# Performance work log

Measured on AMD Instinct MI355X. Metric: run time of the kernel, lower is better.

Reference implementation:

```python
import jax, jax.numpy as jnp
import numpy as np

B, L, C, H, W = 2, 4, 64, 80, 80
DISCRETE_RATIO, DOWNSAMPLE_RATE, NUM_ITER = 0.4, 2, 2


def _conv2d(x, w, b):
    y = jax.lax.conv_general_dilated(x, w, (1, 1), 'SAME',
                                     dimension_numbers=('NCHW', 'OIHW', 'NCHW'))
    return y + b[None, :, None, None]


def _get_transformation_matrix(M, h, w):
    # shift(center) @ [R 0; 0 1] @ shift(-center), then add raw translation (kornia-style)
    R = M[:, :2, :2]
    center = jnp.array([w / 2.0, h / 2.0], M.dtype)
    trans = center[None, :] - jnp.einsum('nij,j->ni', R, center) + M[:, :, 2]
    return jnp.concatenate([R, trans[:, :, None]], axis=2)  # (N,2,3)


def _warp_affine(src, M, mode):
    # src (N,C,h,w); M (N,2,3) maps src pixels -> dst pixels; sample src at M^{-1} @ dst
    # (equivalent to F.affine_grid/grid_sample with align_corners=True, zeros padding)
    N, Cc, h, w = src.shape
    bottom = jnp.tile(jnp.array([[[0.0, 0.0, 1.0]]], src.dtype), (N, 1, 1))
    Minv = jnp.linalg.inv(jnp.concatenate([M, bottom], axis=1))
    yy, xx = jnp.meshgrid(jnp.arange(h, dtype=src.dtype),
                          jnp.arange(w, dtype=src.dtype), indexing='ij')
    pts = jnp.stack([xx.ravel(), yy.ravel(), jnp.ones(h * w, src.dtype)], 0)  # (3,P)
    sp = jnp.einsum('nij,jp->nip', Minv, pts)
    sx, sy = sp[:, 0], sp[:, 1]  # (N,P) source pixel coords
    flat = src.reshape(N, Cc, h * w)

    def gather(ix, iy):
        valid = ((ix >= 0) & (ix < w) & (iy >= 0) & (iy < h)).astype(src.dtype)
        idx = jnp.clip(iy, 0, h - 1) * w + jnp.clip(ix, 0, w - 1)
        vals = jnp.take_along_axis(flat, jnp.broadcast_to(idx[:, None, :], (N, Cc, h * w)), axis=2)
        return vals * valid[:, None, :]

    if mode == 'nearest':
        out = gather(jnp.round(sx).astype(jnp.int32), jnp.round(sy).astype(jnp.int32))
    else:
        x0 = jnp.floor(sx); y0 = jnp.floor(sy)
        fx = (sx - x0)[:, None, :]; fy = (sy - y0)[:, None, :]
        x0 = x0.astype(jnp.int32); y0 = y0.astype(jnp.int32)
        out = (gather(x0, y0) * (1 - fx) * (1 - fy)
               + gather(x0 + 1, y0) * fx * (1 - fy)
               + gather(x0, y0 + 1) * (1 - fx) * fy
               + gather(x0 + 1, y0 + 1) * fx * fy)
    return out.reshape(N, Cc, h, w)


def _forward(x, pairwise_t_matrix, msg_w, msg_b, gates_w, gates_b, can_w, can_b, mlp_w, mlp_b):
    feats = x.reshape(B, L, C, H, W)
    # rows [0,1], cols [0,1,3] of the 4x4 SE(3) matrices; discretize translation
    t = pairwise_t_matrix[..., :2, :][..., jnp.array([0, 1, 3])]  # (B,L,L,2,3)
    t = t.at[..., 2].set(t[..., 2] / (DISCRETE_RATIO * DOWNSAMPLE_RATE))
    T = _get_transformation_matrix(t.reshape(-1, 2, 3), H, W)  # (B*L*L,2,3), flat index (b, j, i)
    mask = _warp_affine(jnp.ones((B * L * L, 1, H, W), x.dtype), T, 'nearest').reshape(B, L, L, 1, H, W)

    for _ in range(NUM_ITER):
        # 'b c h w -> b c w h' + flip(last): coordinate-convention fix (H==W)
        y = jnp.flip(jnp.swapaxes(feats, -1, -2), axis=-1)  # (B,L,C,H,W)
        # warp neighbor j into ego i frame with T[b,j,i]
        src = jnp.broadcast_to(y[:, :, None], (B, L, L, C, H, W)).reshape(-1, C, H, W)
        neighbor = _warp_affine(src, T, 'bilinear')
        ego = jnp.broadcast_to(y[:, None], (B, L, L, C, H, W)).reshape(-1, C, H, W)
        msg = _conv2d(jnp.concatenate([neighbor, ego], axis=1), msg_w, msg_b)
        msg = msg.reshape(B, L, L, C, H, W) * mask
        agg = msg.mean(axis=1)  # 'avg' over neighbors j -> (B,L,C,H,W)
        cat_feat = jnp.concatenate([y, agg], axis=2).reshape(B * L, 2 * C, H, W)
        # single ConvGRU step with zero initial hidden state
        h0 = jnp.zeros((B * L, C, H, W), x.dtype)
        gates = _conv2d(jnp.concatenate([cat_feat, h0], axis=1), gates_w, gates_b)
        reset = jax.nn.sigmoid(gates[:, :C])
        update = jax.nn.sigmoid(gates[:, C:])
        cand = jnp.tanh(_conv2d(jnp.concatenate([cat_feat, reset * h0], axis=1), can_w, can_b))
        h1 = (1.0 - update) * h0 + update * cand
        # undo the coordinate fix: flip(last) then 'c w h -> c h w'
        feats = jnp.swapaxes(jnp.flip(h1.reshape(B, L, C, H, W), axis=-1), -1, -2)

    out = feats[:, 0]  # ego agent of each sample, (B,C,H,W)
    return jnp.einsum('bchw,oc->bhwo', out, mlp_w) + mlp_b  # nn.Linear on channel-last


def setup_inputs() -> dict:
    key = jax.random.key(0)
    ks = jax.random.split(key, 12)
    x = jax.random.normal(ks[0], (B * L, C, H, W), dtype=jnp.float32)
    record_len = jnp.full((B,), L, dtype=jnp.int32)
    # realistic SE(2) pairwise transforms embedded in 4x4 homogeneous matrices
    ang = jax.random.uniform(ks[1], (B, L, L), minval=-0.3, maxval=0.3)
    tx = jax.random.uniform(ks[2], (B, L, L), minval=-8.0, maxval=8.0)
    ty = jax.random.uniform(ks[3], (B, L, L), minval=-8.0, maxval=8.0)
    c, s = jnp.cos(ang), jnp.sin(ang)
    z, o = jnp.zeros_like(ang), jnp.ones_like(ang)
    pairwise_t_matrix = jnp.stack([c, -s, z, tx,
                                   s, c, z, ty,
                                   z, z, o, z,
                                   z, z, z, o], axis=-1).reshape(B, L, L, 4, 4).astype(jnp.float32)
    prior_encoding = jax.random.normal(ks[4], (B * L, 3), dtype=jnp.float32)  # unused by forward
    sc = 0.05
    return {
        'x': x,
        'record_len': record_len,
        'pairwise_t_matrix': pairwise_t_matrix,
        'prior_encoding': prior_encoding,
        'msg_w': jax.random.normal(ks[5], (C, 2 * C, 3, 3), dtype=jnp.float32) * sc,
        'msg_b': jnp.zeros((C,), jnp.float32),
        'gates_w': jax.random.normal(ks[6], (2 * C, 3 * C, 3, 3), dtype=jnp.float32) * sc,
        'gates_b': jnp.zeros((2 * C,), jnp.float32),
        'can_w': jax.random.normal(ks[7], (C, 3 * C, 3, 3), dtype=jnp.float32) * sc,
        'can_b': jnp.zeros((C,), jnp.float32),
        'mlp_w': jax.random.normal(ks[8], (C, C), dtype=jnp.float32) * sc,
        'mlp_b': jnp.zeros((C,), jnp.float32),
    }


def reference(x, record_len, pairwise_t_matrix, prior_encoding,
              msg_w, msg_b, gates_w, gates_b, can_w, can_b, mlp_w, mlp_b):
    # record_len is fixed to L for every sample; prior_encoding is unused by the torch forward
    return _forward(x, pairwise_t_matrix, msg_w, msg_b, gates_w, gates_b,
                    can_w, can_b, mlp_w, mlp_b)
```

## Files before the change

kernel.cpp:

```cpp
#include <hip/hip_runtime.h>
#include <math.h>

#define WD 80
#define HW 6400
#define PW 82
#define PPX 6790
#define NIMG 8
#define NPAIR 32
#define TSTG 960

typedef short bf16x8 __attribute__((ext_vector_type(8)));
typedef float f32x4 __attribute__((ext_vector_type(4)));

__device__ __forceinline__ float bf2f(unsigned short u) {
    return __uint_as_float(((unsigned)u) << 16);
}
__device__ __forceinline__ unsigned short f2bf(float f) {
    unsigned u = __float_as_uint(f);
    u += 0x7fff + ((u >> 16) & 1);
    return (unsigned short)(u >> 16);
}

__device__ __forceinline__ void inv_affine(const float* __restrict__ P, int p, float* a) {
    const float* m = P + p * 16;
    float m00 = m[0], m01 = m[1], m02 = m[3] / 0.8f;
    float m10 = m[4], m11 = m[5], m12 = m[7] / 0.8f;
    float cx = 40.0f, cy = 40.0f;
    float tx = cx - (m00 * cx + m01 * cy) + m02;
    float ty = cy - (m10 * cx + m11 * cy) + m12;
    float id = 1.0f / (m00 * m11 - m01 * m10);
    a[0] =  m11 * id; a[1] = -m01 * id;
    a[3] = -m10 * id; a[4] =  m00 * id;
    a[2] = -(a[0] * tx + a[1] * ty);
    a[5] = -(a[3] * tx + a[4] * ty);
}

__global__ __launch_bounds__(256) void prologue_all(
        const float* __restrict__ P, float* __restrict__ mats, float* __restrict__ mask,
        const float* __restrict__ msg_w, const float* __restrict__ gates_w,
        const float* __restrict__ can_w,
        unsigned short* __restrict__ Wn, unsigned short* __restrict__ We,
        unsigned short* __restrict__ Wu, unsigned short* __restrict__ Wc,
        const float* __restrict__ x, unsigned short* __restrict__ bufs) {
    __shared__ float T[64][81];
    int bx = blockIdx.x;
    if (bx < 243) {
        int idx = bx * 256 + threadIdx.x;
        if (idx >= 24 * 324 * 8) return;
        int g = idx & 7;
        int e = (idx >> 3) % 324;
        int img = idx / (324 * 8);
        int pp;
        if (e < 82)       pp = e;
        else if (e < 164) pp = 81 * PW + (e - 82);
        else if (e < 244) pp = (e - 164 + 1) * PW;
        else              pp = (e - 244 + 1) * PW + 81;
        *(uint4*)(bufs + ((size_t)img * PPX + pp) * 64 + g * 8) = (uint4){0, 0, 0, 0};
        return;
    }
    bx -= 243;
    if (bx < 32) {
        int p = bx;
        float a[6];
        inv_affine(P, p, a);
        if (threadIdx.x < 6) mats[p * 6 + threadIdx.x] = a[threadIdx.x];
        for (int q = threadIdx.x; q < HW; q += blockDim.x) {
            float xx = (float)(q % WD), yy = (float)(q / WD);
            float sx = a[0] * xx + a[1] * yy + a[2];
            float sy = a[3] * xx + a[4] * yy + a[5];
            int ix = (int)rintf(sx), iy = (int)rintf(sy);
            mask[p * HW + q] = (ix >= 0 && ix < WD && iy >= 0 && iy < WD) ? 1.0f : 0.0f;
        }
        return;
    }
    bx -= 32;
    if (bx < 864) {
        int t = bx * 256 + threadIdx.x;
        if (t >= 221184) return;
        const float* src; unsigned short* dst;
        int cin_n, co_off, ci_off, stride, u;
        if (t < 36864)       { src = msg_w;   dst = Wn; cin_n = 64;  co_off = 0;  ci_off = 0;  stride = 1152; u = t; }
        else if (t < 73728)  { src = msg_w;   dst = We; cin_n = 64;  co_off = 0;  ci_off = 64; stride = 1152; u = t - 36864; }
        else if (t < 147456) { src = gates_w; dst = Wu; cin_n = 128; co_off = 64; ci_off = 0;  stride = 1728; u = t - 73728; }
        else                 { src = can_w;   dst = Wc; cin_n = 128; co_off = 0;  ci_off = 0;  stride = 1728; u = t - 147456; }
        int ci = u % cin_n;
        int co = (u / cin_n) & 63;
        int tap = u / (cin_n * 64);
        dst[u] = f2bf(src[(size_t)(co_off + co) * stride + (ci_off + ci) * 9 + tap]);
        return;
    }
    bx -= 864;
    int img = bx / 80, hh = bx % 80;
    int tid = threadIdx.x;
    for (int idx = tid; idx < 64 * 80; idx += 256) {
        int c = idx / 80, ww = idx % 80;
        T[c][ww] = x[((size_t)(img * 64 + c) * 80 + hh) * 80 + ww];
    }
    __syncthreads();
    int b = 79 - hh;
    for (int idx = tid; idx < 80 * 64; idx += 256) {
        int a = idx >> 6, ch = idx & 63;
        bufs[((size_t)img * PPX + (a + 1) * PW + (b + 1)) * 64 + ch] = f2bf(T[ch][a]);
    }
}

__device__ __forceinline__ void stage_t(const unsigned short* __restrict__ src,
                                        int x0, int y0, uint4* bufbase, int tid) {
    const int lane = tid & 63;
    const int wv = tid >> 6;
    for (int c = wv; c < TSTG / 64; c += 4) {
        int s = c * 64 + lane;
        int q = s >> 3;
        int yl = q / 20, xl = q - yl * 20;
        int g = (s & 7) ^ (q & 7);
        const unsigned short* gp = src + ((y0 + yl) * PW + x0 + xl) * 64 + g * 8;
        __builtin_amdgcn_global_load_lds(
            (const __attribute__((address_space(1))) unsigned int*)gp,
            (__attribute__((address_space(3))) unsigned int*)(bufbase + c * 64),
            16, 0, 0);
    }
}

__device__ __forceinline__ void stage_warp(const unsigned short* __restrict__ src,
        const float* __restrict__ am, int x0, int y0, uint4* bufbase, int tid) {
    float a0 = am[0], a1 = am[1], a2 = am[2], a3 = am[3], a4 = am[4], a5 = am[5];
    for (int idx = tid; idx < TSTG; idx += 256) {
        int q = idx >> 3, g = idx & 7;
        int yl = q / 20, xl = q - yl * 20;
        int ux = x0 + xl - 1, uy = y0 + yl - 1;
        uint4 v = {0, 0, 0, 0};
        if ((unsigned)ux < WD && (unsigned)uy < WD) {
            float sx = a0 * ux + a1 * uy + a2;
            float sy = a3 * ux + a4 * uy + a5;
            float fxf = floorf(sx), fyf = floorf(sy);
            float fx = sx - fxf, fy = sy - fyf;
            int ix = (int)fxf, iy = (int)fyf;
            float w00 = (1.f - fx) * (1.f - fy), w10 = fx * (1.f - fy);
            float w01 = (1.f - fx) * fy,         w11 = fx * fy;
            bool vx0 = (unsigned)ix < WD, vx1 = (unsigned)(ix + 1) < WD;
            bool vy0 = (unsigned)iy < WD, vy1 = (unsigned)(iy + 1) < WD;
            if (!(vx0 && vy0)) w00 = 0.f;
            if (!(vx1 && vy0)) w10 = 0.f;
            if (!(vx0 && vy1)) w01 = 0.f;
            if (!(vx1 && vy1)) w11 = 0.f;
            int cx0 = min(max(ix, 0), WD - 1), cx1 = min(max(ix + 1, 0), WD - 1);
            int cy0 = min(max(iy, 0), WD - 1), cy1 = min(max(iy + 1, 0), WD - 1);
            const unsigned short* s8 = src + g * 8;
            uint4 c00 = *(const uint4*)(s8 + ((cy0 + 1) * PW + cx0 + 1) * 64);
            uint4 c10 = *(const uint4*)(s8 + ((cy0 + 1) * PW + cx1 + 1) * 64);
            uint4 c01 = *(const uint4*)(s8 + ((cy1 + 1) * PW + cx0 + 1) * 64);
            uint4 c11 = *(const uint4*)(s8 + ((cy1 + 1) * PW + cx1 + 1) * 64);
            const unsigned short* p00 = (const unsigned short*)&c00;
            const unsigned short* p10 = (const unsigned short*)&c10;
            const unsigned short* p01 = (const unsigned short*)&c01;
            const unsigned short* p11 = (const unsigned short*)&c11;
            unsigned short r8[8];
#pragma unroll
            for (int kk = 0; kk < 8; ++kk) {
                float vv = w00 * bf2f(p00[kk]) + w10 * bf2f(p10[kk])
                         + w01 * bf2f(p01[kk]) + w11 * bf2f(p11[kk]);
                r8[kk] = f2bf(vv);
            }
            v = *(const uint4*)r8;
        }
        bufbase[q * 8 + (g ^ (q & 7))] = v;
    }
}

__device__ __forceinline__ void load_w(const unsigned short* __restrict__ W, int row,
                                       int cinstride, int cin0, int lh, bf16x8* Wf) {
#pragma unroll
    for (int ks = 0; ks < 2; ++ks)
#pragma unroll
        for (int tap = 0; tap < 9; ++tap)
            Wf[ks * 9 + tap] = *(const bf16x8*)(W + (size_t)(tap * 64 + row) * cinstride
                                                + cin0 + ks * 32 + lh * 8);
}

__device__ __forceinline__ void conv_pass4(const uint4* __restrict__ buf, const bf16x8* Wf,
                                           int ll, int lh, f32x4* acc) {
#pragma unroll
    for (int ks = 0; ks < 2; ++ks) {
        const int g = ks * 4 + lh;
#pragma unroll
        for (int tx = 0; tx < 3; ++tx) {
            bf16x8 A[6];
#pragma unroll
            for (int s = 0; s < 6; ++s) {
                int q = s * 20 + tx + ll;
                A[s] = *(const bf16x8*)&buf[q * 8 + (g ^ (q & 7))];
            }
#pragma unroll
            for (int ty = 0; ty < 3; ++ty) {
                bf16x8 B = Wf[ks * 9 + ty * 3 + tx];
#pragma unroll
                for (int r = 0; r < 4; ++r)
                    acc[r] = __builtin_amdgcn_mfma_f32_16x16x32_bf16(A[r + ty], B, acc[r], 0, 0, 0);
            }
        }
    }
}

__global__ __launch_bounds__(256, 2) void msg_agg(const unsigned short* __restrict__ Y,
        const float* __restrict__ mats, const float* __restrict__ mask,
        const unsigned short* __restrict__ Wn, const unsigned short* __restrict__ We,
        const float* __restrict__ bias, unsigned short* __restrict__ Gpad, int only0) {
    __shared__ uint4 lds[2 * TSTG];
    __shared__ float lmask[4][4][16];
    const int tid = threadIdx.x, lane = tid & 63, wv = tid >> 6;
    const int ll = lane & 15, lh = lane >> 4;
    const int x0 = blockIdx.x * 16, y0 = blockIdx.y * 4;
    const int t = blockIdx.z;
    const int b = only0 ? t : (t >> 2), j = only0 ? 0 : (t & 3);
    const int img = only0 ? t * 4 : t;
    const int row = wv * 16 + ll;

    int ps_[4];
#pragma unroll
    for (int i = 0; i < 4; ++i) {
        int k = only0 ? (b * 4 + i) : ((b * 4 + i) * 4 + j);
        ps_[i] = only0 ? k * 4 : k;
    }
    {
        int i = tid >> 6, r = (tid >> 4) & 3, px = tid & 15;
        lmask[i][r][px] = mask[(size_t)ps_[i] * HW + (y0 + r) * WD + x0 + px];
    }
    bf16x8 Wf[18];
    load_w(Wn, row, 64, 0, lh, Wf);
    stage_warp(Y + (size_t)(b * 4 + 0) * PPX * 64, mats + ps_[0] * 6, x0, y0, lds, tid);
    __syncthreads();

    f32x4 tot[4];
#pragma unroll
    for (int r = 0; r < 4; ++r) tot[r] = (f32x4){0.f, 0.f, 0.f, 0.f};

    for (int i = 0; i < 4; ++i) {
        if (i < 3)
            stage_warp(Y + (size_t)(b * 4 + i + 1) * PPX * 64, mats + ps_[i + 1] * 6,
                       x0, y0, lds + ((i + 1) & 1) * TSTG, tid);
        else
            stage_t(Y + (size_t)img * PPX * 64, x0, y0, lds, tid);
        f32x4 acc[4];
#pragma unroll
        for (int r = 0; r < 4; ++r) acc[r] = (f32x4){0.f, 0.f, 0.f, 0.f};
        conv_pass4(lds + (i & 1) * TSTG, Wf, ll, lh, acc);
#pragma unroll
        for (int r = 0; r < 4; ++r)
#pragma unroll
            for (int jj = 0; jj < 4; ++jj)
                tot[r][jj] += lmask[i][r][lh * 4 + jj] * acc[r][jj];
        __syncthreads();
    }

    load_w(We, row, 64, 0, lh, Wf);
    f32x4 acc[4];
#pragma unroll
    for (int r = 0; r < 4; ++r) acc[r] = (f32x4){0.f, 0.f, 0.f, 0.f};
    conv_pass4(lds, Wf, ll, lh, acc);

    float bv = bias[row];
#pragma unroll
    for (int r = 0; r < 4; ++r)
#pragma unroll
        for (int jj = 0; jj < 4; ++jj) {
            int px = lh * 4 + jj;
            float msum = lmask[0][r][px] + lmask[1][r][px] + lmask[2][r][px] + lmask[3][r][px];
            float val = 0.25f * (tot[r][jj] + msum * (acc[r][jj] + bv));
            Gpad[((size_t)t * PPX + (y0 + r + 1) * PW + (x0 + px + 1)) * 64 + row] = f2bf(val);
        }
}

__global__ __launch_bounds__(256, 2) void gru_conv(const unsigned short* __restrict__ Ysrc,
        const unsigned short* __restrict__ Gpad,
        const unsigned short* __restrict__ Wu, const unsigned short* __restrict__ Wc,
        const float* __restrict__ bu, const float* __restrict__ bc,
        unsigned short* __restrict__ Ydst, int only0) {
    __shared__ uint4 lds[2 * TSTG];
    const int tid = threadIdx.x, lane = tid & 63, wv = tid >> 6;
    const int ll = lane & 15, lh = lane >> 4;
    const int x0 = blockIdx.x * 16, y0 = blockIdx.y * 4;
    const int t = blockIdx.z;
    const int img = only0 ? t * 4 : t;
    const int row = wv * 16 + ll;

    stage_t(Ysrc + (size_t)img * PPX * 64, x0, y0, lds, tid);
    stage_t(Gpad + (size_t)t * PPX * 64, x0, y0, lds + TSTG, tid);
    bf16x8 Wf[18];
    load_w(Wu, row, 128, 0, lh, Wf);
    __syncthreads();

    f32x4 aU[4], aC[4];
#pragma unroll
    for (int r = 0; r < 4; ++r) {
        aU[r] = (f32x4){0.f, 0.f, 0.f, 0.f};
        aC[r] = (f32x4){0.f, 0.f, 0.f, 0.f};
    }
    conv_pass4(lds, Wf, ll, lh, aU);
    load_w(Wu, row, 128, 64, lh, Wf);
    conv_pass4(lds + TSTG, Wf, ll, lh, aU);
    load_w(Wc, row, 128, 0, lh, Wf);
    conv_pass4(lds, Wf, ll, lh, aC);
    load_w(Wc, row, 128, 64, lh, Wf);
    conv_pass4(lds + TSTG, Wf, ll, lh, aC);

    float ub = bu[row], cb = bc[row];
#pragma unroll
    for (int r = 0; r < 4; ++r)
#pragma unroll
        for (int jj = 0; jj < 4; ++jj) {
            int x = x0 + lh * 4 + jj;
            float u = 1.f / (1.f + __expf(-(aU[r][jj] + ub)));
            float e2 = __expf(2.f * (aC[r][jj] + cb));
            float c = (e2 - 1.f) / (e2 + 1.f);
            Ydst[((size_t)img * PPX + (y0 + r + 1) * PW + (x + 1)) * 64 + row] = f2bf(u * c);
        }
}

__global__ void final_mlp(const unsigned short* __restrict__ yfin, const float* __restrict__ mw,
                          const float* __restrict__ mb, float* __restrict__ out) {
    int t = blockIdx.x * blockDim.x + threadIdx.x;
    if (t >= 2 * HW * 64) return;
    int o  = t & 63;
    int wv = (t >> 6) % WD;
    int h  = ((t >> 6) / WD) % WD;
    int b  = t / (HW * 64);
    const unsigned short* src = yfin + ((size_t)(b * 4) * PPX + (wv + 1) * PW + (80 - h)) * 64;
    const float* wrow = mw + o * 64;
    float r = mb[o];
#pragma unroll
    for (int c8 = 0; c8 < 8; ++c8) {
        bf16x8 v = *(const bf16x8*)(src + c8 * 8);
#pragma unroll
        for (int k = 0; k < 8; ++k)
            r += bf2f(((const unsigned short*)&v)[k]) * wrow[c8 * 8 + k];
    }
    out[t] = r;
}

extern "C" void kernel_launch(void* const* d_in, const int* in_sizes, int n_in,
                              void* d_out, int out_size, void* d_ws, size_t ws_size,
                              hipStream_t stream) {
    const float* x       = (const float*)d_in[0];
    const float* P       = (const float*)d_in[2];
    const float* msg_w   = (const float*)d_in[4];
    const float* msg_b   = (const float*)d_in[5];
    const float* gates_w = (const float*)d_in[6];
    const float* gates_b = (const float*)d_in[7];
    const float* can_w   = (const float*)d_in[8];
    const float* can_b   = (const float*)d_in[9];
    const float* mlp_w   = (const float*)d_in[10];
    const float* mlp_b   = (const float*)d_in[11];
    float* out = (float*)d_out;

    char* wsb = (char*)d_ws;
    float* mats = (float*)wsb;
    float* mask = (float*)(wsb + 1024);
    unsigned short* Wn = (unsigned short*)(wsb + 820224);
    unsigned short* We = Wn + 36864;
    unsigned short* Wu = We + 36864;
    unsigned short* Wc = Wu + 73728;
    unsigned short* Y0 = Wc + 73728;
    unsigned short* Y1 = Y0 + (size_t)NIMG * PPX * 64;
    unsigned short* Gpad = Y1 + (size_t)NIMG * PPX * 64;

    prologue_all<<<243 + 32 + 864 + 640, 256, 0, stream>>>(P, mats, mask,
        msg_w, gates_w, can_w, Wn, We, Wu, Wc, x, Y0);

    msg_agg<<<dim3(5, 20, 8), 256, 0, stream>>>(Y0, mats, mask, Wn, We, msg_b, Gpad, 0);
    gru_conv<<<dim3(5, 20, 8), 256, 0, stream>>>(Y0, Gpad, Wu, Wc, gates_b + 64, can_b, Y1, 0);

    msg_agg<<<dim3(5, 20, 2), 256, 0, stream>>>(Y1, mats, mask, Wn, We, msg_b, Gpad, 1);
    gru_conv<<<dim3(5, 20, 2), 256, 0, stream>>>(Y1, Gpad, Wu, Wc, gates_b + 64, can_b, Y0, 1);

    final_mlp<<<(2 * HW * 64 + 255) / 256, 256, 0, stream>>>(Y0, mlp_w, mlp_b, out);
}
```

Measured before the change: 239.5 us.

## Make conv kernels loop over tiles with cross-tile LDS prefetch

msg_agg and gru_conv become grid-stride kernels: the first iteration uses 400 blocks that each process two tiles, and the second uses 200 blocks with one tile each. While the current tile is computing, the next tile's warped neighbour data, mask and inputs are staged into a second LDS buffer, so global loads overlap with MFMA work across tile boundaries. In exchange, gru_conv's LDS doubles, which may lower occupancy, and the first iteration launches fewer blocks, which may leave CUs idle on a chip with many compute units.

After: 307.4 us. +28.4%, slower.

```diff
diff --git a/kernel.cpp b/kernel.cpp
--- a/kernel.cpp
+++ b/kernel.cpp
@@ -101,6 +101,21 @@
     for (int idx = tid; idx < 80 * 64; idx += 256) {
         int a = idx >> 6, ch = idx & 63;
         bufs[((size_t)img * PPX + (a + 1) * PW + (b + 1)) * 64 + ch] = f2bf(T[ch][a]);
+    }
+}
+
+struct TileInfo { int x0, y0, t, b, img; int ps[4]; };
+__device__ __forceinline__ void decode_tile(int tt, int only0, TileInfo& ti) {
+    int bx = tt % 5, by = (tt / 5) % 20;
+    ti.t = tt / 100;
+    ti.x0 = bx * 16; ti.y0 = by * 4;
+    int b = only0 ? ti.t : (ti.t >> 2), j = only0 ? 0 : (ti.t & 3);
+    ti.b = b;
+    ti.img = only0 ? ti.t * 4 : ti.t;
+#pragma unroll
+    for (int i = 0; i < 4; ++i) {
+        int k = only0 ? (b * 4 + i) : ((b * 4 + i) * 4 + j);
+        ti.ps[i] = only0 ? k * 4 : k;
     }
 }
 
@@ -204,116 +219,144 @@
 __global__ __launch_bounds__(256, 2) void msg_agg(const unsigned short* __restrict__ Y,
         const float* __restrict__ mats, const float* __restrict__ mask,
         const unsigned short* __restrict__ Wn, const unsigned short* __restrict__ We,
-        const float* __restrict__ bias, unsigned short* __restrict__ Gpad, int only0) {
+        const float* __restrict__ bias, unsigned short* __restrict__ Gpad,
+        int total, int nt, int only0) {
     __shared__ uint4 lds[2 * TSTG];
-    __shared__ float lmask[4][4][16];
+    __shared__ float lmask[2][4][4][16];
     const int tid = threadIdx.x, lane = tid & 63, wv = tid >> 6;
     const int ll = lane & 15, lh = lane >> 4;
-    const int x0 = blockIdx.x * 16, y0 = blockIdx.y * 4;
-    const int t = blockIdx.z;
-    const int b = only0 ? t : (t >> 2), j = only0 ? 0 : (t & 3);
-    const int img = only0 ? t * 4 : t;
     const int row = wv * 16 + ll;
-
-    int ps_[4];
-#pragma unroll
-    for (int i = 0; i < 4; ++i) {
-        int k = only0 ? (b * 4 + i) : ((b * 4 + i) * 4 + j);
-        ps_[i] = only0 ? k * 4 : k;
-    }
-    {
-        int i = tid >> 6, r = (tid >> 4) & 3, px = tid & 15;
-        lmask[i][r][px] = mask[(size_t)ps_[i] * HW + (y0 + r) * WD + x0 + px];
-    }
+    const int mi = tid >> 6, mr = (tid >> 4) & 3, mpx = tid & 15;
+
+    TileInfo ti;
+    decode_tile(blockIdx.x, only0, ti);
+    lmask[0][mi][mr][mpx] = mask[(size_t)ti.ps[mi] * HW + (ti.y0 + mr) * WD + ti.x0 + mpx];
     bf16x8 Wf[18];
     load_w(Wn, row, 64, 0, lh, Wf);
-    stage_warp(Y + (size_t)(b * 4 + 0) * PPX * 64, mats + ps_[0] * 6, x0, y0, lds, tid);
+    stage_warp(Y + (size_t)(ti.b * 4) * PPX * 64, mats + ti.ps[0] * 6, ti.x0, ti.y0, lds, tid);
     __syncthreads();
 
-    f32x4 tot[4];
-#pragma unroll
-    for (int r = 0; r < 4; ++r) tot[r] = (f32x4){0.f, 0.f, 0.f, 0.f};
-
-    for (int i = 0; i < 4; ++i) {
-        if (i < 3)
-            stage_warp(Y + (size_t)(b * 4 + i + 1) * PPX * 64, mats + ps_[i + 1] * 6,
-                       x0, y0, lds + ((i + 1) & 1) * TSTG, tid);
-        else
-            stage_t(Y + (size_t)img * PPX * 64, x0, y0, lds, tid);
+    for (int k = 0; k < nt; ++k) {
+        int tt = blockIdx.x + k * gridDim.x;
+        if (tt >= total) break;
+        const int p = k & 1;
+        decode_tile(tt, only0, ti);
+
+        f32x4 tot[4];
+#pragma unroll
+        for (int r = 0; r < 4; ++r) tot[r] = (f32x4){0.f, 0.f, 0.f, 0.f};
+
+        for (int i = 0; i < 4; ++i) {
+            if (i < 3)
+                stage_warp(Y + (size_t)(ti.b * 4 + i + 1) * PPX * 64, mats + ti.ps[i + 1] * 6,
+                           ti.x0, ti.y0, lds + (p ^ ((i + 1) & 1)) * TSTG, tid);
+            else
+                stage_t(Y + (size_t)ti.img * PPX * 64, ti.x0, ti.y0, lds + p * TSTG, tid);
+            f32x4 acc[4];
+#pragma unroll
+            for (int r = 0; r < 4; ++r) acc[r] = (f32x4){0.f, 0.f, 0.f, 0.f};
+            conv_pass4(lds + (p ^ (i & 1)) * TSTG, Wf, ll, lh, acc);
+#pragma unroll
+            for (int r = 0; r < 4; ++r)
+#pragma unroll
+                for (int jj = 0; jj < 4; ++jj)
+                    tot[r][jj] += lmask[p][i][r][lh * 4 + jj] * acc[r][jj];
+            __syncthreads();
+        }
+
+        load_w(We, row, 64, 0, lh, Wf);
         f32x4 acc[4];
 #pragma unroll
         for (int r = 0; r < 4; ++r) acc[r] = (f32x4){0.f, 0.f, 0.f, 0.f};
-        conv_pass4(lds + (i & 1) * TSTG, Wf, ll, lh, acc);
+        conv_pass4(lds + p * TSTG, Wf, ll, lh, acc);
+
+        int ttn = tt + gridDim.x;
+        if (k + 1 < nt && ttn < total) {
+            TileInfo tn;
+            decode_tile(ttn, only0, tn);
+            stage_warp(Y + (size_t)(tn.b * 4) * PPX * 64, mats + tn.ps[0] * 6,
+                       tn.x0, tn.y0, lds + (p ^ 1) * TSTG, tid);
+            lmask[p ^ 1][mi][mr][mpx] =
+                mask[(size_t)tn.ps[mi] * HW + (tn.y0 + mr) * WD + tn.x0 + mpx];
+            load_w(Wn, row, 64, 0, lh, Wf);
+        }
+
+        float bv = bias[row];
 #pragma unroll
         for (int r = 0; r < 4; ++r)
 #pragma unroll
-            for (int jj = 0; jj < 4; ++jj)
-                tot[r][jj] += lmask[i][r][lh * 4 + jj] * acc[r][jj];
+            for (int jj = 0; jj < 4; ++jj) {
+                int px = lh * 4 + jj;
+                float msum = lmask[p][0][r][px] + lmask[p][1][r][px]
+                           + lmask[p][2][r][px] + lmask[p][3][r][px];
+                float val = 0.25f * (tot[r][jj] + msum * (acc[r][jj] + bv));
+                Gpad[((size_t)ti.t * PPX + (ti.y0 + r + 1) * PW + (ti.x0 + px + 1)) * 64 + row]
+                    = f2bf(val);
+            }
         __syncthreads();
     }
-
-    load_w(We, row, 64, 0, lh, Wf);
-    f32x4 acc[4];
-#pragma unroll
-    for (int r = 0; r < 4; ++r) acc[r] = (f32x4){0.f, 0.f, 0.f, 0.f};
-    conv_pass4(lds, Wf, ll, lh, acc);
-
-    float bv = bias[row];
-#pragma unroll
-    for (int r = 0; r < 4; ++r)
-#pragma unroll
-        for (int jj = 0; jj < 4; ++jj) {
-            int px = lh * 4 + jj;
-            float msum = lmask[0][r][px] + lmask[1][r][px] + lmask[2][r][px] + lmask[3][r][px];
-            float val = 0.25f * (tot[r][jj] + msum * (acc[r][jj] + bv));
-            Gpad[((size_t)t * PPX + (y0 + r + 1) * PW + (x0 + px + 1)) * 64 + row] = f2bf(val);
-        }
 }
 
 __global__ __launch_bounds__(256, 2) void gru_conv(const unsigned short* __restrict__ Ysrc,
         const unsigned short* __restrict__ Gpad,
         const unsigned short* __restrict__ Wu, const unsigned short* __restrict__ Wc,
         const float* __restrict__ bu, const float* __restrict__ bc,
-        unsigned short* __restrict__ Ydst, int only0) {
-    __shared__ uint4 lds[2 * TSTG];
+        unsigned short* __restrict__ Ydst, int total, int nt, int only0) {
+    __shared__ uint4 lds[4 * TSTG];
     const int tid = threadIdx.x, lane = tid & 63, wv = tid >> 6;
     const int ll = lane & 15, lh = lane >> 4;
-    const int x0 = blockIdx.x * 16, y0 = blockIdx.y * 4;
-    const int t = blockIdx.z;
-    const int img = only0 ? t * 4 : t;
     const int row = wv * 16 + ll;
 
-    stage_t(Ysrc + (size_t)img * PPX * 64, x0, y0, lds, tid);
-    stage_t(Gpad + (size_t)t * PPX * 64, x0, y0, lds + TSTG, tid);
+    TileInfo ti;
+    decode_tile(blockIdx.x, only0, ti);
+    stage_t(Ysrc + (size_t)ti.img * PPX * 64, ti.x0, ti.y0, lds, tid);
+    stage_t(Gpad + (size_t)ti.t * PPX * 64, ti.x0, ti.y0, lds + TSTG, tid);
     bf16x8 Wf[18];
     load_w(Wu, row, 128, 0, lh, Wf);
-    __syncthreads();
-
-    f32x4 aU[4], aC[4];
-#pragma unroll
-    for (int r = 0; r < 4; ++r) {
-        aU[r] = (f32x4){0.f, 0.f, 0.f, 0.f};
-        aC[r] = (f32x4){0.f, 0.f, 0.f, 0.f};
-    }
-    conv_pass4(lds, Wf, ll, lh, aU);
-    load_w(Wu, row, 128, 64, lh, Wf);
-    conv_pass4(lds + TSTG, Wf, ll, lh, aU);
-    load_w(Wc, row, 128, 0, lh, Wf);
-    conv_pass4(lds, Wf, ll, lh, aC);
-    load_w(Wc, row, 128, 64, lh, Wf);
-    conv_pass4(lds + TSTG, Wf, ll, lh, aC);
-
-    float ub = bu[row], cb = bc[row];
-#pragma unroll
-    for (int r = 0; r < 4; ++r)
-#pragma unroll
-        for (int jj = 0; jj < 4; ++jj) {
-            int x = x0 + lh * 4 + jj;
-            float u = 1.f / (1.f + __expf(-(aU[r][jj] + ub)));
-            float e2 = __expf(2.f * (aC[r][jj] + cb));
-            float c = (e2 - 1.f) / (e2 + 1.f);
-            Ydst[((size_t)img * PPX + (y0 + r + 1) * PW + (x + 1)) * 64 + row] = f2bf(u * c);
-        }
+
+    for (int k = 0; k < nt; ++k) {
+        int tt = blockIdx.x + k * gridDim.x;
+        if (tt >= total) break;
+        decode_tile(tt, only0, ti);
+        uint4* cur = lds + (k & 1) * 2 * TSTG;
+        __syncthreads();
+        int ttn = tt + gridDim.x;
+        if (k + 1 < nt && ttn < total) {
+            TileInfo tn;
+            decode_tile(ttn, only0, tn);
+            uint4* nxt = lds + ((k + 1) & 1) * 2 * TSTG;
+            stage_t(Ysrc + (size_t)tn.img * PPX * 64, tn.x0, tn.y0, nxt, tid);
+            stage_t(Gpad + (size_t)tn.t * PPX * 64, tn.x0, tn.y0, nxt + TSTG, tid);
+        }
+
+        f32x4 aU[4], aC[4];
+#pragma unroll
+        for (int r = 0; r < 4; ++r) {
+            aU[r] = (f32x4){0.f, 0.f, 0.f, 0.f};
+            aC[r] = (f32x4){0.f, 0.f, 0.f, 0.f};
+        }
+        conv_pass4(cur, Wf, ll, lh, aU);
+        load_w(Wu, row, 128, 64, lh, Wf);
+        conv_pass4(cur + TSTG, Wf, ll, lh, aU);
+        load_w(Wc, row, 128, 0, lh, Wf);
+        conv_pass4(cur, Wf, ll, lh, aC);
+        load_w(Wc, row, 128, 64, lh, Wf);
+        conv_pass4(cur + TSTG, Wf, ll, lh, aC);
+        load_w(Wu, row, 128, 0, lh, Wf);
+
+        float ub = bu[row], cb = bc[row];
+#pragma unroll
+        for (int r = 0; r < 4; ++r)
+#pragma unroll
+            for (int jj = 0; jj < 4; ++jj) {
+                int x = ti.x0 + lh * 4 + jj;
+                float u = 1.f / (1.f + __expf(-(aU[r][jj] + ub)));
+                float e2 = __expf(2.f * (aC[r][jj] + cb));
+                float c = (e2 - 1.f) / (e2 + 1.f);
+                Ydst[((size_t)ti.img * PPX + (ti.y0 + r + 1) * PW + (x + 1)) * 64 + row]
+                    = f2bf(u * c);
+            }
+    }
 }
 
 __global__ void final_mlp(const unsigned short* __restrict__ yfin, const float* __restrict__ mw,
@@ -366,11 +409,11 @@
     prologue_all<<<243 + 32 + 864 + 640, 256, 0, stream>>>(P, mats, mask,
         msg_w, gates_w, can_w, Wn, We, Wu, Wc, x, Y0);
 
-    msg_agg<<<dim3(5, 20, 8), 256, 0, stream>>>(Y0, mats, mask, Wn, We, msg_b, Gpad, 0);
-    gru_conv<<<dim3(5, 20, 8), 256, 0, stream>>>(Y0, Gpad, Wu, Wc, gates_b + 64, can_b, Y1, 0);
-
-    msg_agg<<<dim3(5, 20, 2), 256, 0, stream>>>(Y1, mats, mask, Wn, We, msg_b, Gpad, 1);
-    gru_conv<<<dim3(5, 20, 2), 256, 0, stream>>>(Y1, Gpad, Wu, Wc, gates_b + 64, can_b, Y0, 1);
+    msg_agg<<<400, 256, 0, stream>>>(Y0, mats, mask, Wn, We, msg_b, Gpad, 800, 2, 0);
+    gru_conv<<<400, 256, 0, stream>>>(Y0, Gpad, Wu, Wc, gates_b + 64, can_b, Y1, 800, 2, 0);
+
+    msg_agg<<<200, 256, 0, stream>>>(Y1, mats, mask, Wn, We, msg_b, Gpad, 200, 1, 1);
+    gru_conv<<<200, 256, 0, stream>>>(Y1, Gpad, Wu, Wc, gates_b + 64, can_b, Y0, 200, 1, 1);
 
     final_mlp<<<(2 * HW * 64 + 255) / 256, 256, 0, stream>>>(Y0, mlp_w, mlp_b, out);
 }
```
